# Optimization experiments

Hardware: AMD Instinct MI355X
Metric: run time of the kernel (lower is better)

## Reference

```python
import jax, jax.numpy as jnp
import numpy as np

B, N, M, D = 64, 197, 65, 768


def setup_inputs() -> dict:
    key = jax.random.key(0)
    k1, k2, k3 = jax.random.split(key, 3)
    image = jax.random.normal(k1, (B, N, D), dtype=jnp.float32)
    text = jax.random.normal(k2, (B, M, D), dtype=jnp.float32)
    pm = jax.random.randint(k3, (B, M), 0, 2).astype(jnp.int32)
    pm = pm.at[:, :2].set(0)  # CLS + first real token always valid
    logit_scale = jnp.ones((), dtype=jnp.float32)
    return {"image": image, "text": text, "padding_masks": pm, "logit_scale": logit_scale}


def _ce_with_diag_labels(logits):
    # F.cross_entropy(logits, arange(B)): mean of -log_softmax diag
    return -jnp.mean(jnp.diagonal(jax.nn.log_softmax(logits, axis=-1)))


def reference(image, text, padding_masks, logit_scale):
    # include_cls_token=False: original computes full [B,B,N,M] then slices
    # [:, :, 1:, 1:]; we compute the sliced tokens directly (same math).
    img = image[:, 1:, :]                   # [B, N-1, D]
    txt = text[:, 1:, :]                    # [B, M-1, D]
    pm = padding_masks[:, 1:].astype(bool)  # [B, M-1] True = padded

    # sim[i,j,n,m] = logit_scale * <img_i,n , txt_j,m>
    sim = logit_scale * jnp.einsum('ind,jmd->ijnm', img, txt)  # [B,B,N-1,M-1]

    # Original masks with NaN along mask of batch-row i (broadcast over j,n).
    # logits_per_image: nan_to_num(-inf) -> max over m -> mean over n
    sim_img = jnp.where(pm[:, None, None, :], -jnp.inf, sim)
    logits_per_image = jnp.mean(jnp.max(sim_img, axis=3), axis=2)  # [B,B]

    # logits_per_text: max over n (NaN cols stay NaN) -> nanmean over m.
    # Equivalent masked mean over valid m (mask constant along n).
    max_n = jnp.max(sim, axis=2)                         # [B,B,M-1]
    valid = ~pm                                          # [B,M-1]
    cnt = jnp.sum(valid, axis=1).astype(sim.dtype)       # [B]
    logits_per_text = jnp.sum(
        jnp.where(valid[:, None, :], max_n, 0.0), axis=2
    ) / cnt[:, None]                                     # [B,B]

    loss = 0.5 * (_ce_with_diag_labels(logits_per_image)
                  + _ce_with_diag_labels(logits_per_text))
    targets = jnp.arange(logits_per_image.shape[0], dtype=jnp.int32)
    return loss, logits_per_image, logits_per_text, targets
```

## Files before the change

### kernel.cpp

```cpp
#include <hip/hip_runtime.h>

typedef _Float16 half8 __attribute__((ext_vector_type(8)));
typedef float floatx4 __attribute__((ext_vector_type(4)));
typedef float float4v __attribute__((ext_vector_type(4)));

#define AUNITS (64 * 13 * 24 * 64)
#define TUNITS (64 * 4 * 24 * 64)
#define A_HALFS ((size_t)AUNITS * 8)
#define BJ_HALFS (24 * 4 * 64 * 8)
#define AI_HALFS (13 * 24 * 512)

__device__ __forceinline__ void gl_lds16(const _Float16* g, _Float16* l) {
  __builtin_amdgcn_global_load_lds(
      (const __attribute__((address_space(1))) unsigned int*)g,
      (__attribute__((address_space(3))) unsigned int*)l, 16, 0, 0);
}

__global__ __launch_bounds__(256) void repack(const float* __restrict__ img,
                                              const float* __restrict__ txt,
                                              _Float16* __restrict__ Apk,
                                              _Float16* __restrict__ Bpk) {
  int gid = blockIdx.x * 256 + threadIdx.x;
  const float* src;
  _Float16* dst;
  if (gid < AUNITS) {
    int l = gid & 63, g = gid >> 6;
    int s = g % 24; g /= 24;
    int tau = g % 13; int i = g / 13;
    int n = tau * 16 + (l & 15); if (n > 195) n = 195;
    src = img + (size_t)i * 197 * 768 + (size_t)(n + 1) * 768 + s * 32 + (l >> 4) * 8;
    dst = Apk + (size_t)gid * 8;
  } else {
    int u = gid - AUNITS;
    int l = u & 63, g = u >> 6;
    int ct = g & 3; g >>= 2;
    int s = g % 24; int j = g / 24;
    int m = ct * 16 + (l & 15);
    src = txt + (size_t)j * 65 * 768 + (size_t)(m + 1) * 768 + s * 32 + (l >> 4) * 8;
    dst = Bpk + (size_t)u * 8;
  }
  float4v v0 = *(const float4v*)src;
  float4v v1 = *(const float4v*)(src + 4);
  half8 h;
  h[0] = (_Float16)v0[0]; h[1] = (_Float16)v0[1]; h[2] = (_Float16)v0[2]; h[3] = (_Float16)v0[3];
  h[4] = (_Float16)v1[0]; h[5] = (_Float16)v1[1]; h[6] = (_Float16)v1[2]; h[7] = (_Float16)v1[3];
  *(half8*)dst = h;
}

__global__ __launch_bounds__(512, 2) void sim_kernel(const _Float16* __restrict__ Apk,
                                                     const _Float16* __restrict__ Bpk,
                                                     const int* __restrict__ pm,
                                                     const float* __restrict__ ls,
                                                     float* __restrict__ lpi,
                                                     float* __restrict__ lpt) {
  __shared__ _Float16 Lds[59392];

  const int jb4 = blockIdx.x, i = blockIdx.y;
  const int tid = threadIdx.x;
  const int wave = tid >> 6, lane = tid & 63;
  const int wr = wave >> 2, wc = wave & 3;
  const int NT = 7 - wr;
  const int r16 = lane & 15;
  const int lane8 = lane * 8;

  _Float16* LB = Lds;
  _Float16* LA = Lds + 32768;
  const _Float16* Ag = Apk + (size_t)i * AI_HALFS;
  const _Float16* Bg = Bpk + (size_t)(4 * jb4) * BJ_HALFS + (size_t)(wave & 3) * BJ_HALFS;

  auto stage = [&](int cc) {
    const int buf = cc & 1;
    if (wave < 4) {
#pragma unroll
      for (int k = 0; k < 8; ++k) {
        int sc = k >> 2, ct = k & 3;
        gl_lds16(Bg + (size_t)(2 * cc + sc) * 2048 + ct * 512 + lane8,
                 LB + buf * 16384 + wave * 4096 + sc * 2048 + ct * 512);
      }
    } else {
#pragma unroll
      for (int k = 0; k < 8; ++k) {
        int m = (wave - 4) * 8 + k;
        int tau = m >> 1; if (tau > 12) tau = 12;
        int sc = m & 1;
        gl_lds16(Ag + (size_t)tau * 12288 + (size_t)(2 * cc + sc) * 512 + lane8,
                 LA + buf * 13312 + sc * 6656 + tau * 512);
      }
    }
  };

  stage(0);

  floatx4 acc[7][4];
#pragma unroll
  for (int t = 0; t < 7; ++t)
#pragma unroll
    for (int n = 0; n < 4; ++n)
      acc[t][n] = (floatx4){0.f, 0.f, 0.f, 0.f};

#pragma unroll
  for (int c = 0; c < 12; ++c) {
    asm volatile("s_waitcnt vmcnt(0)" ::: "memory");
    __builtin_amdgcn_s_barrier();
    __builtin_amdgcn_sched_barrier(0);
    if (c < 11) stage(c + 1);

#pragma unroll
    for (int sc = 0; sc < 2; ++sc) {
      half8 b[4];
#pragma unroll
      for (int n = 0; n < 4; ++n) {
        int ct = (n + 2 * wr) & 3;
        b[n] = *(const half8*)(LB + (c & 1) * 16384 + wc * 4096 + sc * 2048 + ct * 512 + lane8);
      }
      half8 a[7];
#pragma unroll
      for (int t = 0; t < 7; ++t)
        if (t < NT)
          a[t] = *(const half8*)(LA + (c & 1) * 13312 + sc * 6656 + (wr * 7 + t) * 512 + lane8);

      __builtin_amdgcn_s_setprio(1);
#pragma unroll
      for (int t = 0; t < 7; ++t)
        if (t < NT) {
#pragma unroll
          for (int n = 0; n < 4; ++n)
            acc[t][n] = __builtin_amdgcn_mfma_f32_16x16x32_f16(a[t], b[n], acc[t][n], 0, 0, 0);
        }
      __builtin_amdgcn_s_setprio(0);
    }
  }

  const float sgl = ls[0];
  int colc[4]; bool msk[4];
#pragma unroll
  for (int n = 0; n < 4; ++n) {
    colc[n] = ((n + 2 * wr) & 3) * 16 + r16;
    msk[n] = pm[i * 65 + 1 + colc[n]] != 0;
  }

  float rowsum = 0.f;
#pragma unroll
  for (int t = 0; t < 7; ++t)
    if (t < NT) {
#pragma unroll
      for (int r = 0; r < 4; ++r) {
        float rm = -__builtin_inff();
#pragma unroll
        for (int n = 0; n < 4; ++n) {
          float v = acc[t][n][r] * sgl;
          rm = fmaxf(rm, msk[n] ? -__builtin_inff() : v);
        }
#pragma unroll
        for (int off = 1; off < 16; off <<= 1)
          rm = fmaxf(rm, __shfl_xor(rm, off, 64));
        bool vrow = (wr == 0) || (t < 5) || ((lane >> 4) == 0);
        rowsum += vrow ? rm : 0.f;
      }
    }
#pragma unroll
  for (int off = 1; off < 64; off <<= 1) rowsum += __shfl_xor(rowsum, off, 64);

  float cm[4];
#pragma unroll
  for (int n = 0; n < 4; ++n) {
    float c = -__builtin_inff();
#pragma unroll
    for (int t = 0; t < 7; ++t)
      if (t < NT) {
#pragma unroll
        for (int r = 0; r < 4; ++r) c = fmaxf(c, acc[t][n][r] * sgl);
      }
    c = fmaxf(c, __shfl_xor(c, 16, 64));
    c = fmaxf(c, __shfl_xor(c, 32, 64));
    cm[n] = c;
  }

  __syncthreads();
  float* colmaxS = (float*)Lds;
  float* wsumS   = (float*)Lds + 512;

  if (lane < 16) {
#pragma unroll
    for (int n = 0; n < 4; ++n) colmaxS[(wc * 2 + wr) * 64 + colc[n]] = cm[n];
  }
  if (lane == 0) wsumS[wc * 2 + wr] = rowsum;
  __syncthreads();

  if (tid < 256) {
    const int j = wave, col = lane;
    bool valid = pm[i * 65 + 1 + col] == 0;
    float v = fmaxf(colmaxS[(j * 2 + 0) * 64 + col], colmaxS[(j * 2 + 1) * 64 + col]);
    float contrib = valid ? v : 0.f;
    float cntv = valid ? 1.f : 0.f;
#pragma unroll
    for (int off = 1; off < 64; off <<= 1) {
      contrib += __shfl_xor(contrib, off, 64);
      cntv += __shfl_xor(cntv, off, 64);
    }
    if (lane == 0) {
      int jout = 4 * jb4 + j;
      lpt[i * 64 + jout] = contrib / cntv;
      lpi[i * 64 + jout] = (wsumS[j * 2] + wsumS[j * 2 + 1]) * 0.0625f / 196.f;
    }
  }
}

__global__ __launch_bounds__(64) void ce_kernel(float* __restrict__ out) {
  const int t = threadIdx.x;
  const float* lpi = out + 1;
  const float* lpt = out + 1 + 4096;

  float mx = -__builtin_inff();
#pragma unroll
  for (int jj = 0; jj < 64; ++jj) mx = fmaxf(mx, lpi[t * 64 + jj]);
  float se = 0.f;
#pragma unroll
  for (int jj = 0; jj < 64; ++jj) se += __expf(lpi[t * 64 + jj] - mx);
  float ci = (mx + __logf(se)) - lpi[t * 64 + t];

  float mx2 = -__builtin_inff();
#pragma unroll
  for (int jj = 0; jj < 64; ++jj) mx2 = fmaxf(mx2, lpt[t * 64 + jj]);
  float se2 = 0.f;
#pragma unroll
  for (int jj = 0; jj < 64; ++jj) se2 += __expf(lpt[t * 64 + jj] - mx2);
  float ct_ = (mx2 + __logf(se2)) - lpt[t * 64 + t];

  float v = ci + ct_;
#pragma unroll
  for (int off = 1; off < 64; off <<= 1) v += __shfl_xor(v, off, 64);
  if (t == 0) out[0] = 0.5f * v / 64.f;
  out[1 + 8192 + t] = (float)t;
}

extern "C" void kernel_launch(void* const* d_in, const int* in_sizes, int n_in,
                              void* d_out, int out_size, void* d_ws, size_t ws_size,
                              hipStream_t stream) {
  const float* image = (const float*)d_in[0];
  const float* text  = (const float*)d_in[1];
  const int*   pm    = (const int*)d_in[2];
  const float* ls    = (const float*)d_in[3];
  float* out = (float*)d_out;

  _Float16* Apk = (_Float16*)d_ws;
  _Float16* Bpk = Apk + A_HALFS;

  repack<<<(AUNITS + TUNITS) / 256, 256, 0, stream>>>(image, text, Apk, Bpk);

  dim3 grid(16, 64);
  sim_kernel<<<grid, 512, 0, stream>>>(Apk, Bpk, pm, ls, out + 1, out + 1 + 4096);
  ce_kernel<<<1, 64, 0, stream>>>(out);
}
```

Baseline: 181.8 us.

## Load B operands directly into registers and keep only A in LDS

Text (B) fragments are no longer staged through LDS. Each wave loads its own B fragments straight from global memory into registers, double-buffered across the two K sub-chunks, so only the image (A) tile remains double-buffered in LDS. A loading is spread over all eight waves, and the wait counts are relaxed to vmcnt(4)/vmcnt(8) so B prefetch can overlap with MFMA work. This cuts LDS use from about 116KB to 52KB and removes the B LDS writes and reads, at the cost of redundant global B loads across the two row-waves and more registers held live.

```diff
diff --git a/kernel.cpp b/kernel.cpp
--- a/kernel.cpp
+++ b/kernel.cpp
@@ -53,7 +53,7 @@
                                                      const float* __restrict__ ls,
                                                      float* __restrict__ lpi,
                                                      float* __restrict__ lpt) {
-  __shared__ _Float16 Lds[59392];
+  __shared__ _Float16 LA[26624];
 
   const int jb4 = blockIdx.x, i = blockIdx.y;
   const int tid = threadIdx.x;
@@ -63,33 +63,21 @@
   const int r16 = lane & 15;
   const int lane8 = lane * 8;
 
-  _Float16* LB = Lds;
-  _Float16* LA = Lds + 32768;
   const _Float16* Ag = Apk + (size_t)i * AI_HALFS;
-  const _Float16* Bg = Bpk + (size_t)(4 * jb4) * BJ_HALFS + (size_t)(wave & 3) * BJ_HALFS;
-
-  auto stage = [&](int cc) {
+  const _Float16* Bgw = Bpk + (size_t)(4 * jb4 + wc) * BJ_HALFS + lane8;
+
+  auto stageA = [&](int cc) {
     const int buf = cc & 1;
-    if (wave < 4) {
-#pragma unroll
-      for (int k = 0; k < 8; ++k) {
-        int sc = k >> 2, ct = k & 3;
-        gl_lds16(Bg + (size_t)(2 * cc + sc) * 2048 + ct * 512 + lane8,
-                 LB + buf * 16384 + wave * 4096 + sc * 2048 + ct * 512);
-      }
-    } else {
-#pragma unroll
-      for (int k = 0; k < 8; ++k) {
-        int m = (wave - 4) * 8 + k;
-        int tau = m >> 1; if (tau > 12) tau = 12;
-        int sc = m & 1;
-        gl_lds16(Ag + (size_t)tau * 12288 + (size_t)(2 * cc + sc) * 512 + lane8,
+#pragma unroll
+    for (int k = 0; k < 4; ++k) {
+      int p = wave + 8 * k;
+      if (p < 26) {
+        int tau = p >> 1, sc = p & 1;
+        gl_lds16(Ag + (size_t)(tau * 24 + 2 * cc + sc) * 512 + lane8,
                  LA + buf * 13312 + sc * 6656 + tau * 512);
       }
     }
   };
-
-  stage(0);
 
   floatx4 acc[7][4];
 #pragma unroll
@@ -98,36 +86,67 @@
     for (int n = 0; n < 4; ++n)
       acc[t][n] = (floatx4){0.f, 0.f, 0.f, 0.f};
 
+  half8 a[2][7];
+  half8 b[2][4];
+
+  stageA(0);
+#pragma unroll
+  for (int n = 0; n < 4; ++n) b[0][n] = *(const half8*)(Bgw + n * 512);
+  __builtin_amdgcn_sched_barrier(0);
+  asm volatile("s_waitcnt vmcnt(4)" ::: "memory");
+  __builtin_amdgcn_s_barrier();
+  __builtin_amdgcn_sched_barrier(0);
+
 #pragma unroll
   for (int c = 0; c < 12; ++c) {
-    asm volatile("s_waitcnt vmcnt(0)" ::: "memory");
-    __builtin_amdgcn_s_barrier();
+    const int buf = c & 1;
+
+#pragma unroll
+    for (int t = 0; t < 7; ++t)
+      if (t < NT) {
+        a[0][t] = *(const half8*)(LA + buf * 13312 +        (wr * 7 + t) * 512 + lane8);
+        a[1][t] = *(const half8*)(LA + buf * 13312 + 6656 + (wr * 7 + t) * 512 + lane8);
+      }
+
+    if (c < 11) stageA(c + 1);
+
+#pragma unroll
+    for (int n = 0; n < 4; ++n)
+      b[1][n] = *(const half8*)(Bgw + (size_t)(2 * c + 1) * 2048 + n * 512);
     __builtin_amdgcn_sched_barrier(0);
-    if (c < 11) stage(c + 1);
-
-#pragma unroll
-    for (int sc = 0; sc < 2; ++sc) {
-      half8 b[4];
-#pragma unroll
-      for (int n = 0; n < 4; ++n) {
-        int ct = (n + 2 * wr) & 3;
-        b[n] = *(const half8*)(LB + (c & 1) * 16384 + wc * 4096 + sc * 2048 + ct * 512 + lane8);
-      }
-      half8 a[7];
-#pragma unroll
-      for (int t = 0; t < 7; ++t)
-        if (t < NT)
-          a[t] = *(const half8*)(LA + (c & 1) * 13312 + sc * 6656 + (wr * 7 + t) * 512 + lane8);
-
-      __builtin_amdgcn_s_setprio(1);
-#pragma unroll
-      for (int t = 0; t < 7; ++t)
-        if (t < NT) {
-#pragma unroll
-          for (int n = 0; n < 4; ++n)
-            acc[t][n] = __builtin_amdgcn_mfma_f32_16x16x32_f16(a[t], b[n], acc[t][n], 0, 0, 0);
-        }
-      __builtin_amdgcn_s_setprio(0);
+
+    __builtin_amdgcn_s_setprio(1);
+#pragma unroll
+    for (int t = 0; t < 7; ++t)
+      if (t < NT) {
+#pragma unroll
+        for (int n = 0; n < 4; ++n)
+          acc[t][n] = __builtin_amdgcn_mfma_f32_16x16x32_f16(a[0][t], b[0][n], acc[t][n], 0, 0, 0);
+      }
+    __builtin_amdgcn_s_setprio(0);
+
+    if (c < 11) {
+#pragma unroll
+      for (int n = 0; n < 4; ++n)
+        b[0][n] = *(const half8*)(Bgw + (size_t)(2 * c + 2) * 2048 + n * 512);
+    }
+    __builtin_amdgcn_sched_barrier(0);
+
+    __builtin_amdgcn_s_setprio(1);
+#pragma unroll
+    for (int t = 0; t < 7; ++t)
+      if (t < NT) {
+#pragma unroll
+        for (int n = 0; n < 4; ++n)
+          acc[t][n] = __builtin_amdgcn_mfma_f32_16x16x32_f16(a[1][t], b[1][n], acc[t][n], 0, 0, 0);
+      }
+    __builtin_amdgcn_s_setprio(0);
+
+    if (c < 11) {
+      __builtin_amdgcn_sched_barrier(0);
+      asm volatile("s_waitcnt vmcnt(8)" ::: "memory");
+      __builtin_amdgcn_s_barrier();
+      __builtin_amdgcn_sched_barrier(0);
     }
   }
 
@@ -135,7 +154,7 @@
   int colc[4]; bool msk[4];
 #pragma unroll
   for (int n = 0; n < 4; ++n) {
-    colc[n] = ((n + 2 * wr) & 3) * 16 + r16;
+    colc[n] = n * 16 + r16;
     msk[n] = pm[i * 65 + 1 + colc[n]] != 0;
   }
 
@@ -177,8 +196,8 @@
   }
 
   __syncthreads();
-  float* colmaxS = (float*)Lds;
-  float* wsumS   = (float*)Lds + 512;
+  float* colmaxS = (float*)LA;
+  float* wsumS   = (float*)LA + 512;
 
   if (lane < 16) {
 #pragma unroll
```

Result: slower. 191.6 us (+5.4%).
